# Optimization experiments

Measured on AMD Instinct MI355X. Metric: run time of the kernel, lower is better.

Reference implementation:

```python
import jax, jax.numpy as jnp
import numpy as np

D_MODEL = 768
NHEAD = 12
DK = D_MODEL // NHEAD
MAX_DIST = 1000.0
FF = 3072
POS_HIDDEN = 32  # hidden width of the relative-position bias MLP
EPS = 1e-5
B, L = 2, 1024


def setup_inputs() -> dict:
    key = jax.random.key(0)
    ks = jax.random.split(key, 24)

    def lin(k, i, o):  # torch-Linear-like init, stored as (in, out)
        return jax.random.uniform(k, (i, o), jnp.float32, -1.0, 1.0) / np.sqrt(i)

    return {
        "src": jax.random.normal(ks[0], (B, L, D_MODEL), jnp.float32),
        "src_x": jax.random.uniform(ks[1], (B, L), jnp.float32) * 1000.0,
        "src_y": jax.random.uniform(ks[2], (B, L), jnp.float32) * 1000.0,
        # attention projections (q,k,v,out)
        "Wq": lin(ks[3], D_MODEL, D_MODEL), "bq": jnp.zeros((D_MODEL,), jnp.float32),
        "Wk": lin(ks[4], D_MODEL, D_MODEL), "bk": jnp.zeros((D_MODEL,), jnp.float32),
        "Wv": lin(ks[5], D_MODEL, D_MODEL), "bv": jnp.zeros((D_MODEL,), jnp.float32),
        "Wo": lin(ks[6], D_MODEL, D_MODEL), "bo": jnp.zeros((D_MODEL,), jnp.float32),
        # relative-position bias MLP: 2 -> POS_HIDDEN -> NHEAD
        "P1": lin(ks[7], 2, POS_HIDDEN), "pb1": jnp.zeros((POS_HIDDEN,), jnp.float32),
        "P2": lin(ks[8], POS_HIDDEN, NHEAD), "pb2": jnp.zeros((NHEAD,), jnp.float32),
        # FFN
        "W1": lin(ks[9], D_MODEL, FF), "b1": jnp.zeros((FF,), jnp.float32),
        "W2": lin(ks[10], FF, D_MODEL), "b2": jnp.zeros((D_MODEL,), jnp.float32),
        # post-LN params
        "g1": jnp.ones((D_MODEL,), jnp.float32), "be1": jnp.zeros((D_MODEL,), jnp.float32),
        "g2": jnp.ones((D_MODEL,), jnp.float32), "be2": jnp.zeros((D_MODEL,), jnp.float32),
    }


def _layernorm(x, g, b):
    m = jnp.mean(x, axis=-1, keepdims=True)
    v = jnp.var(x, axis=-1, keepdims=True)
    return (x - m) * jax.lax.rsqrt(v + EPS) * g + b


def reference(src, src_x, src_y, Wq, bq, Wk, bk, Wv, bv, Wo, bo,
              P1, pb1, P2, pb2, W1, b1, W2, b2, g1, be1, g2, be2):
    b, l, _ = src.shape
    # projections -> (b, h, l, dk)
    q = (src @ Wq + bq).reshape(b, l, NHEAD, DK).transpose(0, 2, 1, 3)
    k = (src @ Wk + bk).reshape(b, l, NHEAD, DK).transpose(0, 2, 1, 3)
    v = (src @ Wv + bv).reshape(b, l, NHEAD, DK).transpose(0, 2, 1, 3)
    # 2D relative positions, clipped and normalized to [-1, 1]
    rx = jnp.clip(src_x[:, :, None] - src_x[:, None, :], -MAX_DIST, MAX_DIST) / MAX_DIST
    ry = jnp.clip(src_y[:, :, None] - src_y[:, None, :], -MAX_DIST, MAX_DIST) / MAX_DIST
    rel = jnp.stack([rx, ry], axis=-1)                        # (b, l, l, 2)
    bias = jax.nn.relu(rel @ P1 + pb1) @ P2 + pb2             # (b, l, l, h)
    bias = bias.transpose(0, 3, 1, 2)                         # (b, h, l, l)
    scores = jnp.einsum('bhqd,bhkd->bhqk', q, k) / np.sqrt(DK).astype(np.float32) + bias
    attn = jax.nn.softmax(scores, axis=-1)
    o = jnp.einsum('bhqk,bhkd->bhqd', attn, v).transpose(0, 2, 1, 3).reshape(b, l, D_MODEL)
    src2 = o @ Wo + bo
    x = _layernorm(src + src2, g1, be1)                       # post-LN residual 1
    ff = jax.nn.relu(x @ W1 + b1) @ W2 + b2                   # FFN
    return _layernorm(x + ff, g2, be2)                        # post-LN residual 2
```

## Files before the change

### kernel.cpp

```cpp
#include <hip/hip_runtime.h>
#include <math.h>

typedef unsigned short ushort_t;
typedef __attribute__((ext_vector_type(8))) short bf16x8;
typedef __attribute__((ext_vector_type(4))) float f32x4;

constexpr int kD      = 768;
constexpr int kNH     = 12;
constexpr int kDK     = 64;
constexpr int kFF     = 3072;
constexpr int kL      = 1024;
constexpr int kRows   = 2048;
constexpr float kEPS  = 1e-5f;

__device__ __forceinline__ ushort_t f2bf(float f) {
    union { float f; unsigned u; } v; v.f = f;
    unsigned r = (v.u + 0x7fffu + ((v.u >> 16) & 1u)) >> 16;
    return (ushort_t)r;
}
__device__ __forceinline__ float bf2f(ushort_t u) {
    union { unsigned u; float f; } v; v.u = ((unsigned)u) << 16; return v.f;
}

#define GL_LDS(gp, lp) __builtin_amdgcn_global_load_lds( \
    (const __attribute__((address_space(1))) void*)(gp), \
    (__attribute__((address_space(3))) void*)(lp), 16, 0, 0)

template<int RELU, int OUTBF, int ADDBIAS>
__device__ __forceinline__ void gemm_body(const ushort_t* __restrict__ A,
                                          const ushort_t* __restrict__ WT,
                                          const float* __restrict__ bias,
                                          void* __restrict__ Cout,
                                          int N, int K, int row0, int col0,
                                          int kbeg, int kend, ushort_t* lds)
{
    const int tid  = threadIdx.x;
    const int lane = tid & 63;
    const int wave = tid >> 6;
    const int wrow = (wave & 1) * 64;
    const int wcol = (wave >> 1) * 64;

    const int srow = wave * 16 + (lane >> 2);
    const int sk   = (lane & 3) * 8;
    const ushort_t* ga0 = A  + (size_t)(row0 + srow)      * K + sk;
    const ushort_t* ga1 = A  + (size_t)(row0 + srow + 64) * K + sk;
    const ushort_t* gb0 = WT + (size_t)(col0 + srow)      * K + sk;
    const ushort_t* gb1 = WT + (size_t)(col0 + srow + 64) * K + sk;

    const int wo = wave * 512;
    const int fl = lane & 15, fq = lane >> 4;

    f32x4 acc[4][4] = {};

    {
        ushort_t* b0 = lds;
        GL_LDS(ga0 + kbeg, b0 + wo);
        GL_LDS(ga1 + kbeg, b0 + 2048 + wo);
        GL_LDS(gb0 + kbeg, b0 + 4096 + wo);
        GL_LDS(gb1 + kbeg, b0 + 4096 + 2048 + wo);
    }
    __syncthreads();

    int cur = 0;
    for (int k0 = kbeg; k0 < kend; k0 += 32) {
        ushort_t* bs = lds + (cur ? 8192 : 0);
        ushort_t* bn = lds + (cur ? 0 : 8192);

        if (k0 + 32 < kend) {
            GL_LDS(ga0 + k0 + 32, bn + wo);
            GL_LDS(ga1 + k0 + 32, bn + 2048 + wo);
            GL_LDS(gb0 + k0 + 32, bn + 4096 + wo);
            GL_LDS(gb1 + k0 + 32, bn + 4096 + 2048 + wo);
        }

        bf16x8 av[4], bv[4];
        #pragma unroll
        for (int i = 0; i < 4; ++i) {
            av[i] = *(const bf16x8*)(bs + (wrow + i * 16 + fl) * 32 + fq * 8);
            bv[i] = *(const bf16x8*)(bs + 4096 + (wcol + i * 16 + fl) * 32 + fq * 8);
        }
        #pragma unroll
        for (int mi = 0; mi < 4; ++mi)
            #pragma unroll
            for (int ni = 0; ni < 4; ++ni)
                acc[mi][ni] = __builtin_amdgcn_mfma_f32_16x16x32_bf16(
                    av[mi], bv[ni], acc[mi][ni], 0, 0, 0);

        __syncthreads();
        cur ^= 1;
    }

    #pragma unroll
    for (int mi = 0; mi < 4; ++mi) {
        const int m = wrow + mi * 16 + fq * 4;
        #pragma unroll
        for (int ni = 0; ni < 4; ++ni) {
            const int n = wcol + ni * 16 + fl;
            const float bb = ADDBIAS ? bias[col0 + n] : 0.f;
            #pragma unroll
            for (int r = 0; r < 4; ++r) {
                float v = acc[mi][ni][r] + bb;
                if (RELU) v = fmaxf(v, 0.f);
                const size_t idx = (size_t)(row0 + m + r) * N + col0 + n;
                if (OUTBF) ((ushort_t*)Cout)[idx] = f2bf(v);
                else       ((float*)Cout)[idx]    = v;
            }
        }
    }
}

template<int RELU, int OUTBF>
__global__ __launch_bounds__(256)
void gemm_kernel(const ushort_t* __restrict__ A, const ushort_t* __restrict__ WT,
                 const float* __restrict__ bias, void* __restrict__ Cout,
                 int N, int K)
{
    __shared__ ushort_t lds[16384];
    gemm_body<RELU, OUTBF, 1>(A, WT, bias, Cout, N, K,
                              blockIdx.y * 128, blockIdx.x * 128, 0, K, lds);
}

__global__ __launch_bounds__(256)
void gemm_splitk_kernel(const ushort_t* __restrict__ A, const ushort_t* __restrict__ WT,
                        float* __restrict__ parts, int N, int K, int kslice)
{
    __shared__ ushort_t lds[16384];
    const int z = blockIdx.z;
    float* out = parts + (size_t)z * kRows * N;
    gemm_body<0, 0, 0>(A, WT, nullptr, out, N, K,
                       blockIdx.y * 128, blockIdx.x * 128,
                       z * kslice, (z + 1) * kslice, lds);
}

__device__ __forceinline__ void wt_tile(const float* __restrict__ src,
                                        ushort_t* __restrict__ dst,
                                        int K, int N, int kt, int nt,
                                        float (*T)[65], int tid)
{
    #pragma unroll
    for (int i = 0; i < 4; ++i) {
        const int e = tid + i * 256;
        const int r = e >> 4;
        const int c = (e & 15) * 4;
        const float4 f = *(const float4*)&src[(size_t)(kt + r) * N + nt + c];
        T[c + 0][r] = f.x; T[c + 1][r] = f.y; T[c + 2][r] = f.z; T[c + 3][r] = f.w;
    }
    __syncthreads();
    #pragma unroll
    for (int i = 0; i < 4; ++i) {
        const int e = tid + i * 256;
        const int n = e >> 4;
        const int kc = (e & 15) * 4;
        ushort4 o;
        o.x = f2bf(T[n][kc + 0]); o.y = f2bf(T[n][kc + 1]);
        o.z = f2bf(T[n][kc + 2]); o.w = f2bf(T[n][kc + 3]);
        *(ushort4*)&dst[(size_t)(nt + n) * K + kt + kc] = o;
    }
}

__global__ __launch_bounds__(256)
void prep_kernel(const float* __restrict__ Wq, const float* __restrict__ Wk,
                 const float* __restrict__ Wv,
                 ushort_t* wqT, ushort_t* wkT, ushort_t* wvT,
                 const float* __restrict__ src, ushort_t* __restrict__ sb)
{
    __shared__ float T[64][65];
    const int bid = blockIdx.x;
    const int tid = threadIdx.x;

    if (bid < 432) {
        const int wz = bid / 144, t = bid - wz * 144;
        const float* s = (wz == 0) ? Wq : (wz == 1) ? Wk : Wv;
        ushort_t*   d = (wz == 0) ? wqT : (wz == 1) ? wkT : wvT;
        wt_tile(s, d, kD, kD, (t % 12) * 64, (t / 12) * 64, T, tid);
    } else {
        const int i = (bid - 432) * 256 + tid;
        const float4 f = ((const float4*)src)[i];
        ushort4 o;
        o.x = f2bf(f.x); o.y = f2bf(f.y); o.z = f2bf(f.z); o.w = f2bf(f.w);
        ((ushort4*)sb)[i] = o;
    }
}

struct BiasSmem {
    float P[32][16];
    float pb2l[12];
    float qxl[16], qyl[16], kxl[64], kyl[64];
    ushort_t Btile[12 * 1024];
};
struct AttnSmem {
    ushort_t Sp[4][16][72];
    ushort_t Ob[4][16][64];
    float    Ll[4][16];
};

__device__ __forceinline__ void bias_body(int bid, BiasSmem& S,
                 const float* __restrict__ sx, const float* __restrict__ sy,
                 const float* __restrict__ P1, const float* __restrict__ pb1,
                 const float* __restrict__ P2, const float* __restrict__ pb2,
                 ushort_t* __restrict__ biasb)
{
    const int b  = bid >> 10;
    const int qt = (bid >> 4) & 63;
    const int kt = bid & 15;
    const int tid = threadIdx.x;

    if (tid < 32) {
        S.P[tid][0] = P1[tid];
        S.P[tid][1] = P1[32 + tid];
        S.P[tid][2] = pb1[tid];
        S.P[tid][3] = 0.f;
    }
    for (int e = tid; e < 384; e += 256) S.P[e / 12][4 + e % 12] = P2[e];
    if (tid < 12) S.pb2l[tid] = pb2[tid];
    if (tid < 16) { S.qxl[tid] = sx[b * kL + qt * 16 + tid];
                    S.qyl[tid] = sy[b * kL + qt * 16 + tid]; }
    if (tid < 64) { S.kxl[tid] = sx[b * kL + kt * 64 + tid];
                    S.kyl[tid] = sy[b * kL + kt * 64 + tid]; }
    __syncthreads();

    const int ri = tid >> 4;
    const int fl = tid & 15;
    const int fq = ri >> 2, r = ri & 3;
    const int lane16 = fq * 16 + fl;
    const float xi = S.qxl[ri], yi = S.qyl[ri];

    float rx[4], ry[4];
    #pragma unroll
    for (int n = 0; n < 4; ++n) {
        const int cj = n * 16 + fl;
        rx[n] = fminf(fmaxf(xi - S.kxl[cj], -1000.f), 1000.f) * 1e-3f;
        ry[n] = fminf(fmaxf(yi - S.kyl[cj], -1000.f), 1000.f) * 1e-3f;
    }

    float acc[4][12] = {};
    #pragma unroll 4
    for (int u = 0; u < 32; ++u) {
        const float4 pc = *(const float4*)&S.P[u][0];
        const float4 w0 = *(const float4*)&S.P[u][4];
        const float4 w1 = *(const float4*)&S.P[u][8];
        const float4 w2 = *(const float4*)&S.P[u][12];
        float t[4];
        #pragma unroll
        for (int n = 0; n < 4; ++n)
            t[n] = fmaxf(fmaf(rx[n], pc.x, fmaf(ry[n], pc.y, pc.z)), 0.f);
        #pragma unroll
        for (int n = 0; n < 4; ++n) {
            acc[n][0]  = fmaf(t[n], w0.x, acc[n][0]);
            acc[n][1]  = fmaf(t[n], w0.y, acc[n][1]);
            acc[n][2]  = fmaf(t[n], w0.z, acc[n][2]);
            acc[n][3]  = fmaf(t[n], w0.w, acc[n][3]);
            acc[n][4]  = fmaf(t[n], w1.x, acc[n][4]);
            acc[n][5]  = fmaf(t[n], w1.y, acc[n][5]);
            acc[n][6]  = fmaf(t[n], w1.z, acc[n][6]);
            acc[n][7]  = fmaf(t[n], w1.w, acc[n][7]);
            acc[n][8]  = fmaf(t[n], w2.x, acc[n][8]);
            acc[n][9]  = fmaf(t[n], w2.y, acc[n][9]);
            acc[n][10] = fmaf(t[n], w2.z, acc[n][10]);
            acc[n][11] = fmaf(t[n], w2.w, acc[n][11]);
        }
    }

    #pragma unroll
    for (int h = 0; h < 12; ++h) {
        const float pb = S.pb2l[h] - 4.0f;
        #pragma unroll
        for (int n = 0; n < 4; ++n)
            S.Btile[h * 1024 + lane16 * 16 + n * 4 + r] = f2bf(acc[n][h] + pb);
    }
    __syncthreads();

    #pragma unroll
    for (int i = 0; i < 6; ++i) {
        const int off = (i * 256 + tid) * 8;
        const int h = off >> 10;
        const int inner = off & 1023;
        ushort_t* dst = biasb +
            (((size_t)(b * kNH + h) * 64 + qt) * 16 + kt) * 1024 + inner;
        *(uint4*)dst = *(const uint4*)&S.Btile[off];
    }
}

constexpr size_t kQkvSmem =
    sizeof(BiasSmem) > 32768 ? sizeof(BiasSmem) : 32768;

__global__ __launch_bounds__(256)
void qkv_bias_kernel(const ushort_t* __restrict__ A,
                     const ushort_t* wq, const ushort_t* wk, const ushort_t* wv,
                     const float* bq, const float* bk, const float* bv,
                     ushort_t* q, ushort_t* k, ushort_t* v,
                     const float* __restrict__ sx, const float* __restrict__ sy,
                     const float* __restrict__ P1, const float* __restrict__ pb1,
                     const float* __restrict__ P2, const float* __restrict__ pb2,
                     ushort_t* __restrict__ biasb)
{
    __shared__ __align__(16) char smem[kQkvSmem];
    const int bid = blockIdx.x;

    if (bid < 288) {
        const int z = bid / 96, rem = bid - z * 96;
        const int bx = rem % 6, by = rem / 6;
        const ushort_t* WT; const float* bias; ushort_t* out;
        if (z == 0)      { WT = wq; bias = bq; out = q; }
        else if (z == 1) { WT = wk; bias = bk; out = k; }
        else             { WT = wv; bias = bv; out = v; }
        gemm_body<0, 1, 1>(A, WT, bias, out, kD, kD,
                           by * 128, bx * 128, 0, kD, (ushort_t*)smem);
    } else {
        bias_body(bid - 288, *(BiasSmem*)smem, sx, sy, P1, pb1, P2, pb2, biasb);
    }
}

__global__ __launch_bounds__(256)
void vtrans_kernel(const ushort_t* __restrict__ vb, ushort_t* __restrict__ vt)
{
    const int bh = blockIdx.x;
    const int b = bh / kNH, h = bh - b * kNH;
    const int j0 = blockIdx.y * 64;
    __shared__ ushort_t T[64][72];

    const int tid = threadIdx.x;
    {
        const int jr = tid & 63;
        const int c0 = (tid >> 6) * 16;
        const ushort_t* sp = vb + (size_t)(b * kL + j0 + jr) * kD + h * kDK + c0;
        uint4 u0 = *(const uint4*)sp;
        uint4 u1 = *(const uint4*)(sp + 8);
        const ushort_t* e0 = (const ushort_t*)&u0;
        const ushort_t* e1 = (const ushort_t*)&u1;
        #pragma unroll
        for (int jj = 0; jj < 8; ++jj) {
            T[c0 + jj][jr]     = e0[jj];
            T[c0 + 8 + jj][jr] = e1[jj];
        }
    }
    __syncthreads();
    {
        const int dr = tid >> 2;
        const int jc = (tid & 3) * 16;
        ushort_t* dp = vt + (size_t)(bh * 64 + dr) * kL + j0 + jc;
        *(uint4*)dp       = *(const uint4*)&T[dr][jc];
        *(uint4*)(dp + 8) = *(const uint4*)&T[dr][jc + 8];
    }
}

constexpr size_t kAttnWtSmem =
    sizeof(AttnSmem) > sizeof(float) * 64 * 65 ? sizeof(AttnSmem)
                                               : sizeof(float) * 64 * 65;

__global__ __launch_bounds__(256)
void attn_wt_kernel(const ushort_t* __restrict__ qg, const ushort_t* __restrict__ kg,
                    const ushort_t* __restrict__ vt, const ushort_t* __restrict__ biasb,
                    ushort_t* __restrict__ og,
                    const float* __restrict__ Wo, const float* __restrict__ W1,
                    const float* __restrict__ W2,
                    ushort_t* woT, ushort_t* w1T, ushort_t* w2T)
{
    __shared__ __align__(16) char smem[kAttnWtSmem];
    const int bid = blockIdx.x;
    const int tid = threadIdx.x;

    if (bid >= 768) {
        float (*T)[65] = (float(*)[65])smem;
        const int t = bid - 768;
        if (t < 144)      wt_tile(Wo, woT, kD,  kD,  (t % 12) * 64, (t / 12) * 64, T, tid);
        else if (t < 720) { const int t2 = t - 144;
                            wt_tile(W1, w1T, kD,  kFF, (t2 % 12) * 64, (t2 / 12) * 64, T, tid); }
        else              { const int t2 = t - 720;
                            wt_tile(W2, w2T, kFF, kD,  (t2 % 48) * 64, (t2 / 48) * 64, T, tid); }
        return;
    }

    AttnSmem& S = *(AttnSmem*)smem;
    const int swz  = (bid & 7) * 96 + (bid >> 3);
    const int bh   = swz >> 5;
    const int qt32 = swz & 31;
    const int b  = bh / kNH, h = bh - b * kNH;
    const int z  = tid >> 6;
    const int qs = z & 1;
    const int kh = z >> 1;
    const int lane = tid & 63;
    const int fl = lane & 15, fq = lane >> 4;
    const int qt = qt32 * 2 + qs;
    const int q0 = qt * 16;
    const int kbeg = kh * 512;

    const size_t qoff = (size_t)(b * kL + q0 + fl) * kD + h * kDK + fq * 8;
    const bf16x8 aq0 = *(const bf16x8*)(qg + qoff);
    const bf16x8 aq1 = *(const bf16x8*)(qg + qoff + 32);

    const ushort_t* kbase = kg + (size_t)(b * kL) * kD + h * kDK + fq * 8;
    const ushort_t* vbase = vt + (size_t)(bh * 64) * kL + fq * 8;
    const ushort_t* btile = biasb +
        ((size_t)(bh * 64 + qt) * 16 + kh * 8) * 1024 + lane * 16;

    f32x4 accO[4] = {};
    float l_part[4] = {};

    bf16x8 kc[4][2];
    uint4 bc0, bc1;
    {
        #pragma unroll
        for (int n = 0; n < 4; ++n) {
            const ushort_t* kr = kbase + (size_t)(kbeg + n * 16 + fl) * kD;
            kc[n][0] = *(const bf16x8*)kr;
            kc[n][1] = *(const bf16x8*)(kr + 32);
        }
        bc0 = *(const uint4*)btile;
        bc1 = *(const uint4*)(btile + 8);
    }

    #pragma unroll 4
    for (int t = 0; t < 8; ++t) {
        const int k0 = kbeg + t * 64;

        bf16x8 vv[4][2];
        #pragma unroll
        for (int n = 0; n < 4; ++n) {
            const ushort_t* vr = vbase + (size_t)(n * 16 + fl) * kL + k0;
            vv[n][0] = *(const bf16x8*)vr;
            vv[n][1] = *(const bf16x8*)(vr + 32);
        }

        f32x4 Sv[4] = {};
        __builtin_amdgcn_s_setprio(1);
        #pragma unroll
        for (int n = 0; n < 4; ++n) {
            Sv[n] = __builtin_amdgcn_mfma_f32_16x16x32_bf16(aq0, kc[n][0], Sv[n], 0, 0, 0);
            Sv[n] = __builtin_amdgcn_mfma_f32_16x16x32_bf16(aq1, kc[n][1], Sv[n], 0, 0, 0);
        }
        __builtin_amdgcn_s_setprio(0);

        bf16x8 kn[4][2];
        uint4 bn0, bn1;
        if (t < 7) {
            #pragma unroll
            for (int n = 0; n < 4; ++n) {
                const ushort_t* kr = kbase + (size_t)(k0 + 64 + n * 16 + fl) * kD;
                kn[n][0] = *(const bf16x8*)kr;
                kn[n][1] = *(const bf16x8*)(kr + 32);
            }
            bn0 = *(const uint4*)(btile + (t + 1) * 1024);
            bn1 = *(const uint4*)(btile + (t + 1) * 1024 + 8);
        }

        ushort_t bu[16];
        *(uint4*)&bu[0] = bc0;
        *(uint4*)&bu[8] = bc1;

        #pragma unroll
        for (int n = 0; n < 4; ++n)
            #pragma unroll
            for (int r = 0; r < 4; ++r) {
                const float e = __expf(fmaf(Sv[n][r], 0.125f, bf2f(bu[n * 4 + r])));
                Sv[n][r] = e;
                l_part[r] += e;
            }

        #pragma unroll
        for (int n = 0; n < 4; ++n)
            #pragma unroll
            for (int r = 0; r < 4; ++r)
                S.Sp[z][fq * 4 + r][n * 16 + fl] = f2bf(Sv[n][r]);

        const bf16x8 ap0 = *(const bf16x8*)&S.Sp[z][fl][fq * 8];
        const bf16x8 ap1 = *(const bf16x8*)&S.Sp[z][fl][32 + fq * 8];
        __builtin_amdgcn_s_setprio(1);
        #pragma unroll
        for (int n = 0; n < 4; ++n) {
            accO[n] = __builtin_amdgcn_mfma_f32_16x16x32_bf16(ap0, vv[n][0], accO[n], 0, 0, 0);
            accO[n] = __builtin_amdgcn_mfma_f32_16x16x32_bf16(ap1, vv[n][1], accO[n], 0, 0, 0);
        }
        __builtin_amdgcn_s_setprio(0);

        if (t < 7) {
            #pragma unroll
            for (int n = 0; n < 4; ++n) { kc[n][0] = kn[n][0]; kc[n][1] = kn[n][1]; }
            bc0 = bn0; bc1 = bn1;
        }
    }

    float l_full[4], inv[4];
    #pragma unroll
    for (int r = 0; r < 4; ++r) {
        float l = l_part[r];
        l += __shfl_xor(l, 1, 16);
        l += __shfl_xor(l, 2, 16);
        l += __shfl_xor(l, 4, 16);
        l += __shfl_xor(l, 8, 16);
        l_full[r] = l;
        inv[r] = 1.0f / l;
    }

    #pragma unroll
    for (int n = 0; n < 4; ++n)
        #pragma unroll
        for (int r = 0; r < 4; ++r)
            S.Ob[z][fq * 4 + r][n * 16 + fl] = f2bf(accO[n][r] * inv[r]);
    if (fl == 0) {
        #pragma unroll
        for (int r = 0; r < 4; ++r)
            S.Ll[z][fq * 4 + r] = l_full[r];
    }
    __syncthreads();

    {
        const int ri = tid >> 3;
        const int d0 = (tid & 7) * 8;
        const int qs2 = ri >> 4, rr = ri & 15;
        const int z0 = qs2, z1 = 2 + qs2;
        const float w0 = S.Ll[z0][rr], w1 = S.Ll[z1][rr];
        const float winv = 1.0f / (w0 + w1);
        const float c0 = w0 * winv, c1 = w1 * winv;

        ushort_t o[8];
        #pragma unroll
        for (int j = 0; j < 8; ++j)
            o[j] = f2bf(fmaf(c0, bf2f(S.Ob[z0][rr][d0 + j]),
                             c1 * bf2f(S.Ob[z1][rr][d0 + j])));
        ushort_t* dp = og + (size_t)(b * kL + qt32 * 32 + ri) * kD + h * kDK + d0;
        *(uint4*)dp = *(const uint4*)o;
    }
}

template<int NPART, int DUAL>
__global__ __launch_bounds__(256)
void ln_kernel(const float* __restrict__ a, const float* __restrict__ parts,
               const float* __restrict__ bias,
               const float* __restrict__ g, const float* __restrict__ be,
               float* __restrict__ out, ushort_t* __restrict__ out_bf)
{
    const int row = blockIdx.x;
    const int tid = threadIdx.x;
    const float* pa = a + (size_t)row * kD;
    constexpr size_t NTOK = (size_t)kRows * kD;

    float v[3];
    float s = 0.f, sq = 0.f;
    #pragma unroll
    for (int i = 0; i < 3; ++i) {
        const int d = tid + i * 256;
        float t = pa[d] + bias[d];
        #pragma unroll
        for (int p = 0; p < NPART; ++p)
            t += parts[p * NTOK + (size_t)row * kD + d];
        v[i] = t;
        s  += t;
        sq += t * t;
    }
    #pragma unroll
    for (int off = 32; off > 0; off >>= 1) {
        s  += __shfl_down(s, off);
        sq += __shfl_down(sq, off);
    }
    __shared__ float bs[4], bq2[4];
    if ((tid & 63) == 0) { bs[tid >> 6] = s; bq2[tid >> 6] = sq; }
    __syncthreads();
    const float ts = bs[0] + bs[1] + bs[2] + bs[3];
    const float tq = bq2[0] + bq2[1] + bq2[2] + bq2[3];
    const float invn = 1.0f / (float)kD;
    const float mean = ts * invn;
    const float var  = tq * invn - mean * mean;
    const float rstd = rsqrtf(var + kEPS);

    float* po = out + (size_t)row * kD;
    #pragma unroll
    for (int i = 0; i < 3; ++i) {
        const int d = tid + i * 256;
        const float o = (v[i] - mean) * rstd * g[d] + be[d];
        po[d] = o;
        if (DUAL) out_bf[(size_t)row * kD + d] = f2bf(o);
    }
}

extern "C" void kernel_launch(void* const* d_in, const int* in_sizes, int n_in,
                              void* d_out, int out_size, void* d_ws, size_t ws_size,
                              hipStream_t stream)
{
    const float* src = (const float*)d_in[0];
    const float* sx  = (const float*)d_in[1];
    const float* sy  = (const float*)d_in[2];
    const float* Wq  = (const float*)d_in[3];  const float* bq  = (const float*)d_in[4];
    const float* Wk  = (const float*)d_in[5];  const float* bk  = (const float*)d_in[6];
    const float* Wv  = (const float*)d_in[7];  const float* bv  = (const float*)d_in[8];
    const float* Wo  = (const float*)d_in[9];  const float* bo  = (const float*)d_in[10];
    const float* P1  = (const float*)d_in[11]; const float* pb1 = (const float*)d_in[12];
    const float* P2  = (const float*)d_in[13]; const float* pb2 = (const float*)d_in[14];
    const float* W1  = (const float*)d_in[15]; const float* b1  = (const float*)d_in[16];
    const float* W2  = (const float*)d_in[17]; const float* b2  = (const float*)d_in[18];
    const float* g1  = (const float*)d_in[19]; const float* be1 = (const float*)d_in[20];
    const float* g2  = (const float*)d_in[21]; const float* be2 = (const float*)d_in[22];

    constexpr size_t W768  = 768u * 768u;
    constexpr size_t W3072 = 768u * 3072u;
    constexpr size_t NTOK  = (size_t)kRows * kD;

    ushort_t* wsu = (ushort_t*)d_ws;
    ushort_t* wqT = wsu;
    ushort_t* wkT = wqT + W768;
    ushort_t* wvT = wkT + W768;
    ushort_t* qb  = wvT + W768;
    ushort_t* kb  = qb + NTOK;
    ushort_t* vb  = kb + NTOK;
    ushort_t* sb  = vb + NTOK;
    ushort_t* vtb = sb + NTOK;
    ushort_t* biasb = vtb + NTOK;
    float*    xb    = (float*)(biasb + W768 + 2 * W3072);
    ushort_t* h1bf  = (ushort_t*)(xb + NTOK);
    ushort_t* xbf   = qb;

    const size_t h1off   = (size_t)(h1bf - wsu);
    const size_t bigNeed = (h1off + 20 * NTOK + W768 + 2 * W3072) * 2;
    const bool   big     = ws_size >= bigNeed;

    float*    s2p;
    float*    ff2p;
    ushort_t* scratch;
    int npWo, npFF;
    if (big) {
        s2p     = (float*)h1bf;
        ff2p    = (float*)(h1bf + 8 * NTOK);
        scratch = h1bf + 20 * NTOK;
        npWo = 4; npFF = 6;
    } else {
        s2p     = (float*)h1bf;
        ff2p    = (float*)(h1bf + 4 * NTOK);
        scratch = (ushort_t*)(ff2p + 3 * NTOK);
        npWo = 2; npFF = 3;
    }
    ushort_t* woT2 = scratch;
    ushort_t* w1T2 = woT2 + W768;
    ushort_t* w2T2 = w1T2 + W3072;

    const dim3 blk(256);

    prep_kernel<<<dim3(1968), blk, 0, stream>>>(Wq, Wk, Wv, wqT, wkT, wvT, src, sb);

    qkv_bias_kernel<<<dim3(2336), blk, 0, stream>>>(
        sb, wqT, wkT, wvT, bq, bk, bv, qb, kb, vb,
        sx, sy, P1, pb1, P2, pb2, biasb);

    vtrans_kernel<<<dim3(2 * kNH, kL / 64), blk, 0, stream>>>(vb, vtb);

    attn_wt_kernel<<<dim3(2064), blk, 0, stream>>>(
        qb, kb, vtb, biasb, sb, Wo, W1, W2, woT2, w1T2, w2T2);

    gemm_splitk_kernel<<<dim3(kD / 128, kRows / 128, npWo), blk, 0, stream>>>(
        sb, woT2, s2p, kD, kD, kD / npWo);

    if (big) ln_kernel<4, 1><<<dim3(kRows), blk, 0, stream>>>(src, s2p, bo, g1, be1, xb, xbf);
    else     ln_kernel<2, 1><<<dim3(kRows), blk, 0, stream>>>(src, s2p, bo, g1, be1, xb, xbf);

    gemm_kernel<1, 1><<<dim3(kFF / 128, kRows / 128), blk, 0, stream>>>(
        xbf, w1T2, b1, h1bf, kFF, kD);

    gemm_splitk_kernel<<<dim3(kD / 128, kRows / 128, npFF), blk, 0, stream>>>(
        h1bf, w2T2, ff2p, kD, kFF, kFF / npFF);

    if (big) ln_kernel<6, 0><<<dim3(kRows), blk, 0, stream>>>(xb, ff2p, b2, g2, be2,
                                                              (float*)d_out, nullptr);
    else     ln_kernel<3, 0><<<dim3(kRows), blk, 0, stream>>>(xb, ff2p, b2, g2, be2,
                                                              (float*)d_out, nullptr);
}
```

Before: 274.6 us.

## Fuse V transpose into QKV GEMM epilogue and stage bf16 stores through LDS

The V projection GEMM now writes its bf16 output already transposed into the per-head V^T layout. It does this by staging the tile in LDS and then writing coalesced 16-byte rows, which removes the separate vtrans kernel launch and its extra read and write of V. The bf16 epilogue for Q, K and the FFN1 GEMM also stages through LDS with padded rows, so stores become vectorized instead of scattered 2-byte writes. In exchange LDS per block grows slightly and there is an extra barrier plus LDS round trip in the epilogue.

```diff
diff --git a/kernel.cpp b/kernel.cpp
--- a/kernel.cpp
+++ b/kernel.cpp
@@ -26,7 +26,7 @@
     (const __attribute__((address_space(1))) void*)(gp), \
     (__attribute__((address_space(3))) void*)(lp), 16, 0, 0)
 
-template<int RELU, int OUTBF, int ADDBIAS>
+template<int RELU, int OUTMODE, int ADDBIAS>
 __device__ __forceinline__ void gemm_body(const ushort_t* __restrict__ A,
                                           const ushort_t* __restrict__ WT,
                                           const float* __restrict__ bias,
@@ -90,41 +90,75 @@
         cur ^= 1;
     }
 
-    #pragma unroll
-    for (int mi = 0; mi < 4; ++mi) {
-        const int m = wrow + mi * 16 + fq * 4;
-        #pragma unroll
-        for (int ni = 0; ni < 4; ++ni) {
-            const int n = wcol + ni * 16 + fl;
-            const float bb = ADDBIAS ? bias[col0 + n] : 0.f;
+    if (OUTMODE == 0) {
+        #pragma unroll
+        for (int mi = 0; mi < 4; ++mi) {
+            const int m = wrow + mi * 16 + fq * 4;
             #pragma unroll
-            for (int r = 0; r < 4; ++r) {
-                float v = acc[mi][ni][r] + bb;
-                if (RELU) v = fmaxf(v, 0.f);
-                const size_t idx = (size_t)(row0 + m + r) * N + col0 + n;
-                if (OUTBF) ((ushort_t*)Cout)[idx] = f2bf(v);
-                else       ((float*)Cout)[idx]    = v;
+            for (int ni = 0; ni < 4; ++ni) {
+                const int n = wcol + ni * 16 + fl;
+                const float bb = ADDBIAS ? bias[col0 + n] : 0.f;
+                #pragma unroll
+                for (int r = 0; r < 4; ++r) {
+                    float v = acc[mi][ni][r] + bb;
+                    if (RELU) v = fmaxf(v, 0.f);
+                    ((float*)Cout)[(size_t)(row0 + m + r) * N + col0 + n] = v;
+                }
             }
         }
-    }
-}
-
-template<int RELU, int OUTBF>
+    } else {
+        ushort_t* T = lds;
+        #pragma unroll
+        for (int mi = 0; mi < 4; ++mi) {
+            const int m = wrow + mi * 16 + fq * 4;
+            #pragma unroll
+            for (int ni = 0; ni < 4; ++ni) {
+                const int n = wcol + ni * 16 + fl;
+                const float bb = ADDBIAS ? bias[col0 + n] : 0.f;
+                #pragma unroll
+                for (int r = 0; r < 4; ++r) {
+                    float v = acc[mi][ni][r] + bb;
+                    if (RELU) v = fmaxf(v, 0.f);
+                    if (OUTMODE == 1) T[(m + r) * 136 + n] = f2bf(v);
+                    else              T[n * 136 + (m + r)] = f2bf(v);
+                }
+            }
+        }
+        __syncthreads();
+        const int row = tid >> 1;
+        const int seg = tid & 1;
+        const ushort_t* sp = T + row * 136 + seg * 64;
+        ushort_t* dp;
+        if (OUTMODE == 1) {
+            dp = (ushort_t*)Cout + (size_t)(row0 + row) * N + col0 + seg * 64;
+        } else {
+            const int bb2 = row0 >> 10;
+            const int c   = col0 + row;
+            const int vtr = (bb2 * kNH + (c >> 6)) * kDK + (c & 63);
+            dp = (ushort_t*)Cout + (size_t)vtr * kL + (row0 & 1023) + seg * 64;
+        }
+        #pragma unroll
+        for (int i = 0; i < 8; ++i)
+            *(uint4*)(dp + i * 8) = *(const uint4*)(sp + i * 8);
+    }
+}
+
+template<int RELU, int OUTMODE>
 __global__ __launch_bounds__(256)
 void gemm_kernel(const ushort_t* __restrict__ A, const ushort_t* __restrict__ WT,
                  const float* __restrict__ bias, void* __restrict__ Cout,
                  int N, int K)
 {
-    __shared__ ushort_t lds[16384];
-    gemm_body<RELU, OUTBF, 1>(A, WT, bias, Cout, N, K,
-                              blockIdx.y * 128, blockIdx.x * 128, 0, K, lds);
+    __shared__ ushort_t lds[17408];
+    gemm_body<RELU, OUTMODE, 1>(A, WT, bias, Cout, N, K,
+                                blockIdx.y * 128, blockIdx.x * 128, 0, K, lds);
 }
 
 __global__ __launch_bounds__(256)
 void gemm_splitk_kernel(const ushort_t* __restrict__ A, const ushort_t* __restrict__ WT,
                         float* __restrict__ parts, int N, int K, int kslice)
 {
-    __shared__ ushort_t lds[16384];
+    __shared__ ushort_t lds[17408];
     const int z = blockIdx.z;
     float* out = parts + (size_t)z * kRows * N;
     gemm_body<0, 0, 0>(A, WT, nullptr, out, N, K,
@@ -282,13 +316,13 @@
 }
 
 constexpr size_t kQkvSmem =
-    sizeof(BiasSmem) > 32768 ? sizeof(BiasSmem) : 32768;
+    sizeof(BiasSmem) > 34816 ? sizeof(BiasSmem) : 34816;
 
 __global__ __launch_bounds__(256)
 void qkv_bias_kernel(const ushort_t* __restrict__ A,
                      const ushort_t* wq, const ushort_t* wk, const ushort_t* wv,
                      const float* bq, const float* bk, const float* bv,
-                     ushort_t* q, ushort_t* k, ushort_t* v,
+                     ushort_t* q, ushort_t* k, ushort_t* vt,
                      const float* __restrict__ sx, const float* __restrict__ sy,
                      const float* __restrict__ P1, const float* __restrict__ pb1,
                      const float* __restrict__ P2, const float* __restrict__ pb2,
@@ -300,47 +334,17 @@
     if (bid < 288) {
         const int z = bid / 96, rem = bid - z * 96;
         const int bx = rem % 6, by = rem / 6;
-        const ushort_t* WT; const float* bias; ushort_t* out;
-        if (z == 0)      { WT = wq; bias = bq; out = q; }
-        else if (z == 1) { WT = wk; bias = bk; out = k; }
-        else             { WT = wv; bias = bv; out = v; }
-        gemm_body<0, 1, 1>(A, WT, bias, out, kD, kD,
-                           by * 128, bx * 128, 0, kD, (ushort_t*)smem);
+        if (z == 0)
+            gemm_body<0, 1, 1>(A, wq, bq, q,  kD, kD,
+                               by * 128, bx * 128, 0, kD, (ushort_t*)smem);
+        else if (z == 1)
+            gemm_body<0, 1, 1>(A, wk, bk, k,  kD, kD,
+                               by * 128, bx * 128, 0, kD, (ushort_t*)smem);
+        else
+            gemm_body<0, 2, 1>(A, wv, bv, vt, kD, kD,
+                               by * 128, bx * 128, 0, kD, (ushort_t*)smem);
     } else {
         bias_body(bid - 288, *(BiasSmem*)smem, sx, sy, P1, pb1, P2, pb2, biasb);
-    }
-}
-
-__global__ __launch_bounds__(256)
-void vtrans_kernel(const ushort_t* __restrict__ vb, ushort_t* __restrict__ vt)
-{
-    const int bh = blockIdx.x;
-    const int b = bh / kNH, h = bh - b * kNH;
-    const int j0 = blockIdx.y * 64;
-    __shared__ ushort_t T[64][72];
-
-    const int tid = threadIdx.x;
-    {
-        const int jr = tid & 63;
-        const int c0 = (tid >> 6) * 16;
-        const ushort_t* sp = vb + (size_t)(b * kL + j0 + jr) * kD + h * kDK + c0;
-        uint4 u0 = *(const uint4*)sp;
-        uint4 u1 = *(const uint4*)(sp + 8);
-        const ushort_t* e0 = (const ushort_t*)&u0;
-        const ushort_t* e1 = (const ushort_t*)&u1;
-        #pragma unroll
-        for (int jj = 0; jj < 8; ++jj) {
-            T[c0 + jj][jr]     = e0[jj];
-            T[c0 + 8 + jj][jr] = e1[jj];
-        }
-    }
-    __syncthreads();
-    {
-        const int dr = tid >> 2;
-        const int jc = (tid & 3) * 16;
-        ushort_t* dp = vt + (size_t)(bh * 64 + dr) * kL + j0 + jc;
-        *(uint4*)dp       = *(const uint4*)&T[dr][jc];
-        *(uint4*)(dp + 8) = *(const uint4*)&T[dr][jc + 8];
     }
 }
 
@@ -637,10 +641,8 @@
     prep_kernel<<<dim3(1968), blk, 0, stream>>>(Wq, Wk, Wv, wqT, wkT, wvT, src, sb);
 
     qkv_bias_kernel<<<dim3(2336), blk, 0, stream>>>(
-        sb, wqT, wkT, wvT, bq, bk, bv, qb, kb, vb,
+        sb, wqT, wkT, wvT, bq, bk, bv, qb, kb, vtb,
         sx, sy, P1, pb1, P2, pb2, biasb);
-
-    vtrans_kernel<<<dim3(2 * kNH, kL / 64), blk, 0, stream>>>(vb, vtb);
 
     attn_wt_kernel<<<dim3(2064), blk, 0, stream>>>(
         qb, kb, vtb, biasb, sb, Wo, W1, W2, woT2, w1T2, w2T2);
```

Measured after the change: 278.1 us. About the same (+1.3%).
